# Optimization experiments

Hardware: AMD Instinct MI355X
Metric: run time of the kernel (lower is better)

The kernel has to match this reference:

```python
import jax, jax.numpy as jnp
import numpy as np
import math

B, C, H, W = 4, 256, 64, 64
NUM_HEADS = 4
GROUPS = 32
EPS = 1e-5


def setup_inputs() -> dict:
    key = jax.random.key(0)
    ks = jax.random.split(key, 7)
    x = jax.random.normal(ks[0], (B, C, H, W), dtype=jnp.float32)
    gn_w = jax.random.normal(ks[1], (C,), dtype=jnp.float32) * 0.02 + 1.0
    gn_b = jax.random.normal(ks[2], (C,), dtype=jnp.float32) * 0.02
    qkv_w = jax.random.normal(ks[3], (3 * C, C), dtype=jnp.float32) * (1.0 / math.sqrt(C))
    qkv_b = jax.random.normal(ks[4], (3 * C,), dtype=jnp.float32) * 0.02
    proj_w = jax.random.normal(ks[5], (C, C), dtype=jnp.float32) * (1.0 / math.sqrt(C))
    proj_b = jax.random.normal(ks[6], (C,), dtype=jnp.float32) * 0.02
    return {"x": x, "gn_w": gn_w, "gn_b": gn_b, "qkv_w": qkv_w,
            "qkv_b": qkv_b, "proj_w": proj_w, "proj_b": proj_b}


def reference(x, gn_w, gn_b, qkv_w, qkv_b, proj_w, proj_b):
    b, c, h, w = x.shape
    t = h * w
    xf = x.reshape(b, c, t)                       # [B, C, T]

    # GroupNorm(32, C) over (channels-in-group, T)
    xg = xf.reshape(b, GROUPS, c // GROUPS, t)
    mean = jnp.mean(xg, axis=(2, 3), keepdims=True)
    var = jnp.var(xg, axis=(2, 3), keepdims=True)
    xn = ((xg - mean) * jax.lax.rsqrt(var + EPS)).reshape(b, c, t)
    xn = xn * gn_w[None, :, None] + gn_b[None, :, None]

    # 1x1 conv QKV: [B, 3C, T]
    qkv = jnp.einsum('oc,bct->bot', qkv_w, xn) + qkv_b[None, :, None]

    nh = NUM_HEADS
    ch = c // nh
    q, k, v = jnp.split(qkv, 3, axis=1)           # each [B, H*ch, T]
    q = q.reshape(b * nh, ch, t)
    k = k.reshape(b * nh, ch, t)
    v = v.reshape(b * nh, ch, t)

    scale = 1.0 / math.sqrt(math.sqrt(ch))
    logits = jnp.einsum('bct,bcs->bts', q * scale, k * scale)   # [B*H, T, T]
    weight = jax.nn.softmax(logits.astype(jnp.float32), axis=-1).astype(logits.dtype)
    a = jnp.einsum('bts,bcs->bct', weight, v)     # [B*H, ch, T]
    a = a.reshape(b, c, t)

    hproj = jnp.einsum('oc,bct->bot', proj_w, a) + proj_b[None, :, None]
    return (xf + hproj).reshape(b, c, h, w)
```

## Files before the change

### kernel.cpp

```cpp
#include <hip/hip_runtime.h>
#include <cstdint>
#include <cstddef>

#define TT 4096
#define CCH 256

typedef __attribute__((ext_vector_type(8))) short short8;
typedef __attribute__((ext_vector_type(4))) float f32x4;

__device__ __forceinline__ float bf2f(unsigned int u){
  union { unsigned int i; float f; } v; v.i = u << 16; return v.f;
}
__device__ __forceinline__ unsigned short f2bf(float f){
  unsigned int x = __float_as_uint(f);
  x += 0x7fffu + ((x >> 16) & 1u);
  return (unsigned short)(x >> 16);
}
__device__ __forceinline__ unsigned short f2bf_t(float f){
  return (unsigned short)(__float_as_uint(f) >> 16);
}
__device__ __forceinline__ int sw(int row, int col){
  return (row << 6) + ((((col >> 3) ^ (row & 7)) << 3)) + (col & 7);
}

__global__ __launch_bounds__(256)
void wconv_gn(const float* __restrict__ qkv_w, const float* __restrict__ proj_w,
              const float* __restrict__ x,
              unsigned short* __restrict__ wq_bf, unsigned short* __restrict__ wp_bf,
              float* __restrict__ stats){
  int bid = blockIdx.x, tid = threadIdx.x;
  if (bid < 256){
    const float* src = (bid < 192) ? qkv_w : proj_w;
    unsigned short* dst = (bid < 192) ? wq_bf : wp_bf;
    int i = (bid < 192 ? bid : bid - 192) * 256 + tid;
    float4 u = *(const float4*)(src + (size_t)i * 4);
    ushort4 r; r.x = f2bf(u.x); r.y = f2bf(u.y); r.z = f2bf(u.z); r.w = f2bf(u.w);
    *(ushort4*)(dst + (size_t)i * 4) = r;
    return;
  }
  int sg = bid - 256;
  const float4* p = (const float4*)(x + (size_t)sg * 32768);
  float s = 0.f, sq = 0.f;
  #pragma unroll
  for (int it = 0; it < 32; ++it){
    float4 u = p[it * 256 + tid];
    s  += u.x + u.y + u.z + u.w;
    sq += u.x*u.x + u.y*u.y + u.z*u.z + u.w*u.w;
  }
  #pragma unroll
  for (int off = 32; off >= 1; off >>= 1){
    s  += __shfl_down(s, off);
    sq += __shfl_down(sq, off);
  }
  __shared__ float ls[4], lq[4];
  int w_ = tid >> 6, lane = tid & 63;
  if (lane == 0){ ls[w_] = s; lq[w_] = sq; }
  __syncthreads();
  if (tid == 0){
    float S = ls[0]+ls[1]+ls[2]+ls[3];
    float Q = lq[0]+lq[1]+lq[2]+lq[3];
    float mean = S * (1.f/32768.f);
    float var  = Q * (1.f/32768.f) - mean*mean;
    stats[2*sg]   = mean;
    stats[2*sg+1] = rsqrtf(var + 1e-5f);
  }
}

__global__ __launch_bounds__(256)
void gn_apply_t(const float* __restrict__ x, const float* __restrict__ gw,
                const float* __restrict__ gb, const float* __restrict__ stats,
                unsigned short* __restrict__ xnT){
  __shared__ unsigned short t_lds[64][72];
  int tid = threadIdx.x;
  int t0 = blockIdx.x << 6, c0 = blockIdx.y << 6, b = blockIdx.z;
  int t4 = (tid & 15) << 2, cr = tid >> 4;
  #pragma unroll
  for (int pass = 0; pass < 4; ++pass){
    int cl = (pass << 4) + cr;
    int c = c0 + cl;
    int sg = (b << 5) | (c >> 3);
    float mean = stats[2*sg], rstd = stats[2*sg+1];
    float sc = gw[c] * rstd;
    float sh = gb[c] - mean * sc;
    float4 u = *(const float4*)(x + ((size_t)(b*CCH + c))*TT + t0 + t4);
    t_lds[t4+0][cl] = f2bf(u.x*sc + sh);
    t_lds[t4+1][cl] = f2bf(u.y*sc + sh);
    t_lds[t4+2][cl] = f2bf(u.z*sc + sh);
    t_lds[t4+3][cl] = f2bf(u.w*sc + sh);
  }
  __syncthreads();
  #pragma unroll
  for (int pass = 0; pass < 2; ++pass){
    int chunk = (pass << 8) + tid;
    int row = chunk >> 3, c8 = (chunk & 7) << 3;
    *(uint4*)(xnT + ((size_t)b*TT + t0 + row)*256 + c0 + c8) = *(const uint4*)&t_lds[row][c8];
  }
}

__global__ __launch_bounds__(256)
void qkv_mfma(const unsigned short* __restrict__ wb, const float* __restrict__ bias,
              const unsigned short* __restrict__ xnT,
              unsigned short* __restrict__ qT, unsigned short* __restrict__ kT,
              unsigned short* __restrict__ vO){
  __shared__ unsigned short x_lds[4096];
  int tid = threadIdx.x;
  int w = tid >> 6, lane = tid & 63, quad = lane >> 4, l15 = lane & 15;
  int t0 = blockIdx.x << 6, o0 = blockIdx.y << 6, b = blockIdx.z;
  const unsigned short* xb = xnT + (size_t)b * TT * 256;
  const unsigned short* wrow = wb + (size_t)(o0 + (w << 4) + l15) * 256;
  f32x4 acc[4];
  #pragma unroll
  for (int nt = 0; nt < 4; ++nt) acc[nt] = (f32x4){0.f,0.f,0.f,0.f};
  for (int ks = 0; ks < 4; ++ks){
    int k0 = ks << 6;
    __syncthreads();
    #pragma unroll
    for (int pass = 0; pass < 2; ++pass){
      int chunk = (pass << 8) + tid;
      int row = chunk >> 3, c8 = (chunk & 7) << 3;
      *(uint4*)&x_lds[sw(row, c8)] = *(const uint4*)(xb + (size_t)(t0 + row)*256 + k0 + c8);
    }
    __syncthreads();
    short8 wa0 = *(const short8*)(wrow + k0 + (quad << 3));
    short8 wa1 = *(const short8*)(wrow + k0 + 32 + (quad << 3));
    #pragma unroll
    for (int nt = 0; nt < 4; ++nt){
      short8 xb0 = *(const short8*)&x_lds[sw((nt << 4) + l15, quad << 3)];
      short8 xb1 = *(const short8*)&x_lds[sw((nt << 4) + l15, 32 + (quad << 3))];
      acc[nt] = __builtin_amdgcn_mfma_f32_16x16x32_bf16(wa0, xb0, acc[nt], 0, 0, 0);
      acc[nt] = __builtin_amdgcn_mfma_f32_16x16x32_bf16(wa1, xb1, acc[nt], 0, 0, 0);
    }
  }
  int sec = blockIdx.y >> 2, h = blockIdx.y & 3, bh = (b << 2) | h;
  float bs[4];
  #pragma unroll
  for (int r = 0; r < 4; ++r) bs[r] = bias[o0 + (w << 4) + (quad << 2) + r];
  __syncthreads();
  if (sec < 2){
    float qsc = (sec == 0) ? 0.125f * 1.44269504f : 1.0f;
    #pragma unroll
    for (int nt = 0; nt < 4; ++nt){
      ushort4 pk;
      pk.x = f2bf((acc[nt][0] + bs[0]) * qsc);
      pk.y = f2bf((acc[nt][1] + bs[1]) * qsc);
      pk.z = f2bf((acc[nt][2] + bs[2]) * qsc);
      pk.w = f2bf((acc[nt][3] + bs[3]) * qsc);
      *(ushort4*)&x_lds[sw((nt << 4) + l15, (w << 4) + (quad << 2))] = pk;
    }
    __syncthreads();
    unsigned short* dst = (sec == 0) ? qT : kT;
    #pragma unroll
    for (int pass = 0; pass < 2; ++pass){
      int chunk = (pass << 8) + tid;
      int row = chunk >> 3, c8 = (chunk & 7) << 3;
      *(uint4*)(dst + ((size_t)bh*TT + t0 + row)*64 + c8) = *(const uint4*)&x_lds[sw(row, c8)];
    }
  } else {
    #pragma unroll
    for (int nt = 0; nt < 4; ++nt)
      #pragma unroll
      for (int r = 0; r < 4; ++r)
        x_lds[sw((w << 4) + (quad << 2) + r, (nt << 4) + l15)] = f2bf(acc[nt][r] + bs[r]);
    __syncthreads();
    #pragma unroll
    for (int pass = 0; pass < 2; ++pass){
      int chunk = (pass << 8) + tid;
      int row = chunk >> 3, c8 = (chunk & 7) << 3;
      *(uint4*)(vO + ((size_t)bh*64 + row)*TT + t0 + c8) = *(const uint4*)&x_lds[sw(row, c8)];
    }
  }
}

__global__ __launch_bounds__(256, 4)
void attn7(const unsigned short* __restrict__ qT, const unsigned short* __restrict__ kT,
           const unsigned short* __restrict__ vO, unsigned short* __restrict__ aT){
  __shared__ __align__(16) unsigned short k_lds[4096];
  __shared__ __align__(16) unsigned short v_lds[4096];
  __shared__ __align__(16) unsigned short p_lds[4096];
  int tid = threadIdx.x;
  int w = tid >> 6, lane = tid & 63, quad = lane >> 4, l15 = lane & 15;
  int bh = blockIdx.x & 15, qt6 = blockIdx.x >> 4;
  int t0 = qt6 << 6;
  const unsigned short* qg = qT + (size_t)bh * TT * 64;
  const unsigned short* kg = kT + (size_t)bh * TT * 64;
  const unsigned short* vg = vO + (size_t)bh * 64 * TT;
  int tw = t0 + (w << 4);

  int row0 = tid >> 3, c80 = (tid & 7) << 3;
  int row1 = row0 + 32;
  int soff0 = sw(row0, c80), soff1 = sw(row1, c80);

  short8 qf[2];
  qf[0] = *(const short8*)(qg + (size_t)(tw + l15)*64 + (quad << 3));
  qf[1] = *(const short8*)(qg + (size_t)(tw + l15)*64 + 32 + (quad << 3));

  f32x4 o_acc[4];
  #pragma unroll
  for (int ct = 0; ct < 4; ++ct) o_acc[ct] = (f32x4){0.f,0.f,0.f,0.f};
  float m_ = -1e30f, l_ = 0.f;

  uint4 kr0 = *(const uint4*)(kg + (size_t)row0*64 + c80);
  uint4 kr1 = *(const uint4*)(kg + (size_t)row1*64 + c80);
  uint4 vr0 = *(const uint4*)(vg + (size_t)row0*TT + c80);
  uint4 vr1 = *(const uint4*)(vg + (size_t)row1*TT + c80);

  for (int st = 0; st < 64; ++st){
    __syncthreads();
    *(uint4*)&k_lds[soff0] = kr0;
    *(uint4*)&k_lds[soff1] = kr1;
    *(uint4*)&v_lds[soff0] = vr0;
    *(uint4*)&v_lds[soff1] = vr1;
    if (st < 63){
      int sn = (st + 1) << 6;
      kr0 = *(const uint4*)(kg + (size_t)(sn + row0)*64 + c80);
      kr1 = *(const uint4*)(kg + (size_t)(sn + row1)*64 + c80);
      vr0 = *(const uint4*)(vg + (size_t)row0*TT + sn + c80);
      vr1 = *(const uint4*)(vg + (size_t)row1*TT + sn + c80);
    }
    __syncthreads();
    f32x4 sv[4];
    #pragma unroll
    for (int mt = 0; mt < 4; ++mt){
      short8 ka0 = *(const short8*)&k_lds[sw((mt << 4) + l15, quad << 3)];
      short8 ka1 = *(const short8*)&k_lds[sw((mt << 4) + l15, 32 + (quad << 3))];
      f32x4 z = (f32x4){0.f,0.f,0.f,0.f};
      z = __builtin_amdgcn_mfma_f32_16x16x32_bf16(ka0, qf[0], z, 0, 0, 0);
      z = __builtin_amdgcn_mfma_f32_16x16x32_bf16(ka1, qf[1], z, 0, 0, 0);
      sv[mt] = z;
    }
    float rm = -1e30f;
    #pragma unroll
    for (int mt = 0; mt < 4; ++mt)
      #pragma unroll
      for (int r = 0; r < 4; ++r) rm = fmaxf(rm, sv[mt][r]);
    rm = fmaxf(rm, __shfl_xor(rm, 16));
    rm = fmaxf(rm, __shfl_xor(rm, 32));
    float mnew = fmaxf(m_, rm);
    float alpha = exp2f(m_ - mnew);
    float rs = 0.f;
    int prow = (w << 4) + l15;
    #pragma unroll
    for (int mt = 0; mt < 4; ++mt){
      float p0 = exp2f(sv[mt][0] - mnew);
      float p1 = exp2f(sv[mt][1] - mnew);
      float p2 = exp2f(sv[mt][2] - mnew);
      float p3 = exp2f(sv[mt][3] - mnew);
      rs += (p0 + p1) + (p2 + p3);
      ushort4 pk; pk.x = f2bf_t(p0); pk.y = f2bf_t(p1); pk.z = f2bf_t(p2); pk.w = f2bf_t(p3);
      *(ushort4*)&p_lds[sw(prow, (mt << 4) + (quad << 2))] = pk;
    }
    rs += __shfl_xor(rs, 16);
    rs += __shfl_xor(rs, 32);
    l_ = l_*alpha + rs;
    m_ = mnew;
    #pragma unroll
    for (int ct = 0; ct < 4; ++ct)
      #pragma unroll
      for (int r = 0; r < 4; ++r) o_acc[ct][r] *= alpha;
    short8 pb0 = *(const short8*)&p_lds[sw(prow, quad << 3)];
    short8 pb1 = *(const short8*)&p_lds[sw(prow, 32 + (quad << 3))];
    #pragma unroll
    for (int ct = 0; ct < 4; ++ct){
      short8 va0 = *(const short8*)&v_lds[sw((ct << 4) + l15, quad << 3)];
      short8 va1 = *(const short8*)&v_lds[sw((ct << 4) + l15, 32 + (quad << 3))];
      o_acc[ct] = __builtin_amdgcn_mfma_f32_16x16x32_bf16(va0, pb0, o_acc[ct], 0, 0, 0);
      o_acc[ct] = __builtin_amdgcn_mfma_f32_16x16x32_bf16(va1, pb1, o_acc[ct], 0, 0, 0);
    }
  }
  __syncthreads();
  float ir = 1.f / l_;
  int prow = (w << 4) + l15;
  #pragma unroll
  for (int ct = 0; ct < 4; ++ct){
    ushort4 ok;
    ok.x = f2bf(o_acc[ct][0] * ir);
    ok.y = f2bf(o_acc[ct][1] * ir);
    ok.z = f2bf(o_acc[ct][2] * ir);
    ok.w = f2bf(o_acc[ct][3] * ir);
    *(ushort4*)&p_lds[sw(prow, (ct << 4) + (quad << 2))] = ok;
  }
  __syncthreads();
  size_t abase = ((size_t)(bh >> 2)*TT + t0)*256 + (size_t)(bh & 3)*64;
  #pragma unroll
  for (int pass = 0; pass < 2; ++pass){
    int chunk = (pass << 8) + tid;
    int row = chunk >> 3, c8 = (chunk & 7) << 3;
    *(uint4*)(aT + abase + (size_t)row*256 + c8) = *(const uint4*)&p_lds[sw(row, c8)];
  }
}

__global__ __launch_bounds__(256)
void proj_mfma(const unsigned short* __restrict__ wb, const float* __restrict__ bias,
               const unsigned short* __restrict__ aT, const float* __restrict__ x,
               float* __restrict__ out){
  __shared__ unsigned short x_lds[4096];
  int tid = threadIdx.x;
  int w = tid >> 6, lane = tid & 63, quad = lane >> 4, l15 = lane & 15;
  int t0 = blockIdx.x << 6, o0 = blockIdx.y << 6, b = blockIdx.z;
  const unsigned short* xb = aT + (size_t)b * TT * 256;
  const unsigned short* wrow = wb + (size_t)(o0 + (w << 4) + l15) * 256;
  f32x4 acc[4];
  #pragma unroll
  for (int nt = 0; nt < 4; ++nt) acc[nt] = (f32x4){0.f,0.f,0.f,0.f};
  for (int ks = 0; ks < 4; ++ks){
    int k0 = ks << 6;
    __syncthreads();
    #pragma unroll
    for (int pass = 0; pass < 2; ++pass){
      int chunk = (pass << 8) + tid;
      int row = chunk >> 3, c8 = (chunk & 7) << 3;
      *(uint4*)&x_lds[sw(row, c8)] = *(const uint4*)(xb + (size_t)(t0 + row)*256 + k0 + c8);
    }
    __syncthreads();
    short8 wa0 = *(const short8*)(wrow + k0 + (quad << 3));
    short8 wa1 = *(const short8*)(wrow + k0 + 32 + (quad << 3));
    #pragma unroll
    for (int nt = 0; nt < 4; ++nt){
      short8 xb0 = *(const short8*)&x_lds[sw((nt << 4) + l15, quad << 3)];
      short8 xb1 = *(const short8*)&x_lds[sw((nt << 4) + l15, 32 + (quad << 3))];
      acc[nt] = __builtin_amdgcn_mfma_f32_16x16x32_bf16(wa0, xb0, acc[nt], 0, 0, 0);
      acc[nt] = __builtin_amdgcn_mfma_f32_16x16x32_bf16(wa1, xb1, acc[nt], 0, 0, 0);
    }
  }
  #pragma unroll
  for (int r = 0; r < 4; ++r){
    int o = o0 + (w << 4) + (quad << 2) + r;
    float bsv = bias[o];
    #pragma unroll
    for (int nt = 0; nt < 4; ++nt){
      size_t idx = ((size_t)(b*CCH + o))*TT + t0 + (nt << 4) + l15;
      out[idx] = acc[nt][r] + bsv + x[idx];
    }
  }
}

extern "C" void kernel_launch(void* const* d_in, const int* in_sizes, int n_in,
                              void* d_out, int out_size, void* d_ws, size_t ws_size,
                              hipStream_t stream){
  const float* x      = (const float*)d_in[0];
  const float* gn_w   = (const float*)d_in[1];
  const float* gn_b   = (const float*)d_in[2];
  const float* qkv_w  = (const float*)d_in[3];
  const float* qkv_b  = (const float*)d_in[4];
  const float* proj_w = (const float*)d_in[5];
  const float* proj_b = (const float*)d_in[6];
  float* out = (float*)d_out;

  float* stats = (float*)d_ws;
  unsigned short* wq_bf = (unsigned short*)(stats + 1024);
  unsigned short* wp_bf = wq_bf + (size_t)768*256;
  unsigned short* xnT   = wp_bf + (size_t)256*256;
  unsigned short* qT    = xnT + (size_t)4*TT*256;
  unsigned short* kT    = qT  + (size_t)16*TT*64;
  unsigned short* vO    = kT  + (size_t)16*TT*64;
  unsigned short* aT    = vO  + (size_t)16*64*TT;

  wconv_gn<<<384, 256, 0, stream>>>(qkv_w, proj_w, x, wq_bf, wp_bf, stats);
  gn_apply_t<<<dim3(64, 4, 4), 256, 0, stream>>>(x, gn_w, gn_b, stats, xnT);
  qkv_mfma<<<dim3(64, 12, 4), 256, 0, stream>>>(wq_bf, qkv_b, xnT, qT, kT, vO);
  attn7<<<1024, 256, 0, stream>>>(qT, kT, vO, aT);
  proj_mfma<<<dim3(64, 4, 4), 256, 0, stream>>>(wp_bf, proj_b, aT, x, out);
}
```

Baseline: 247.8 us.

## Streamline attention softmax with lazy rescale, MFMA row sums and permlane reductions

Reworks the online-softmax inner loop of the attention kernel. The running max is only updated, and the accumulators rescaled, when any lane's new max exceeds the old by more than a threshold, chosen wave-wide via ballot. The row sum of P is computed with an MFMA against a ones vector instead of VALU adds and shuffles. Cross-lane max uses permlane swap instructions, P is packed with a hardware bf16 convert, and MFMA phases get raised scheduling priority. This cuts VALU and shuffle work, but the lazy max lets exponents grow up to 2^8 before rescaling and adds a branch.

Result: faster. 239.3 us (-3.5%).

```diff
diff --git a/kernel.cpp b/kernel.cpp
--- a/kernel.cpp
+++ b/kernel.cpp
@@ -21,6 +21,21 @@
 }
 __device__ __forceinline__ int sw(int row, int col){
   return (row << 6) + ((((col >> 3) ^ (row & 7)) << 3)) + (col & 7);
+}
+__device__ __forceinline__ float bfly_max16(float x){
+  unsigned a = __float_as_uint(x), b = a;
+  asm("v_permlane16_swap_b32 %0, %1" : "+v"(a), "+v"(b));
+  return fmaxf(__uint_as_float(a), __uint_as_float(b));
+}
+__device__ __forceinline__ float bfly_max32(float x){
+  unsigned a = __float_as_uint(x), b = a;
+  asm("v_permlane32_swap_b32 %0, %1" : "+v"(a), "+v"(b));
+  return fmaxf(__uint_as_float(a), __uint_as_float(b));
+}
+__device__ __forceinline__ unsigned cvt_pk_bf16(float lo, float hi){
+  unsigned r;
+  asm("v_cvt_pk_bf16_f32 %0, %1, %2" : "=v"(r) : "v"(lo), "v"(hi));
+  return r;
 }
 
 __global__ __launch_bounds__(256)
@@ -194,6 +209,10 @@
   qf[0] = *(const short8*)(qg + (size_t)(tw + l15)*64 + (quad << 3));
   qf[1] = *(const short8*)(qg + (size_t)(tw + l15)*64 + 32 + (quad << 3));
 
+  short8 ones;
+  #pragma unroll
+  for (int i = 0; i < 8; ++i) ones[i] = (short)0x3F80;
+
   f32x4 o_acc[4];
   #pragma unroll
   for (int ct = 0; ct < 4; ++ct) o_acc[ct] = (f32x4){0.f,0.f,0.f,0.f};
@@ -203,6 +222,8 @@
   uint4 kr1 = *(const uint4*)(kg + (size_t)row1*64 + c80);
   uint4 vr0 = *(const uint4*)(vg + (size_t)row0*TT + c80);
   uint4 vr1 = *(const uint4*)(vg + (size_t)row1*TT + c80);
+
+  int prow = (w << 4) + l15;
 
   for (int st = 0; st < 64; ++st){
     __syncthreads();
@@ -219,6 +240,7 @@
     }
     __syncthreads();
     f32x4 sv[4];
+    __builtin_amdgcn_s_setprio(1);
     #pragma unroll
     for (int mt = 0; mt < 4; ++mt){
       short8 ka0 = *(const short8*)&k_lds[sw((mt << 4) + l15, quad << 3)];
@@ -228,37 +250,40 @@
       z = __builtin_amdgcn_mfma_f32_16x16x32_bf16(ka1, qf[1], z, 0, 0, 0);
       sv[mt] = z;
     }
-    float rm = -1e30f;
-    #pragma unroll
-    for (int mt = 0; mt < 4; ++mt)
+    __builtin_amdgcn_s_setprio(0);
+    float rm = fmaxf(fmaxf(sv[0][0], sv[0][1]), fmaxf(sv[0][2], sv[0][3]));
+    #pragma unroll
+    for (int mt = 1; mt < 4; ++mt)
+      rm = fmaxf(rm, fmaxf(fmaxf(sv[mt][0], sv[mt][1]), fmaxf(sv[mt][2], sv[mt][3])));
+    rm = bfly_max16(rm);
+    rm = bfly_max32(rm);
+    float alpha = 1.0f;
+    if (__ballot(rm > m_ + 8.0f)){
+      float mnew = fmaxf(m_, rm);
+      alpha = exp2f(m_ - mnew);
+      m_ = mnew;
       #pragma unroll
-      for (int r = 0; r < 4; ++r) rm = fmaxf(rm, sv[mt][r]);
-    rm = fmaxf(rm, __shfl_xor(rm, 16));
-    rm = fmaxf(rm, __shfl_xor(rm, 32));
-    float mnew = fmaxf(m_, rm);
-    float alpha = exp2f(m_ - mnew);
-    float rs = 0.f;
-    int prow = (w << 4) + l15;
+      for (int ct = 0; ct < 4; ++ct)
+        #pragma unroll
+        for (int r = 0; r < 4; ++r) o_acc[ct][r] *= alpha;
+    }
     #pragma unroll
     for (int mt = 0; mt < 4; ++mt){
-      float p0 = exp2f(sv[mt][0] - mnew);
-      float p1 = exp2f(sv[mt][1] - mnew);
-      float p2 = exp2f(sv[mt][2] - mnew);
-      float p3 = exp2f(sv[mt][3] - mnew);
-      rs += (p0 + p1) + (p2 + p3);
-      ushort4 pk; pk.x = f2bf_t(p0); pk.y = f2bf_t(p1); pk.z = f2bf_t(p2); pk.w = f2bf_t(p3);
-      *(ushort4*)&p_lds[sw(prow, (mt << 4) + (quad << 2))] = pk;
-    }
-    rs += __shfl_xor(rs, 16);
-    rs += __shfl_xor(rs, 32);
-    l_ = l_*alpha + rs;
-    m_ = mnew;
-    #pragma unroll
-    for (int ct = 0; ct < 4; ++ct)
-      #pragma unroll
-      for (int r = 0; r < 4; ++r) o_acc[ct][r] *= alpha;
+      float p0 = exp2f(sv[mt][0] - m_);
+      float p1 = exp2f(sv[mt][1] - m_);
+      float p2 = exp2f(sv[mt][2] - m_);
+      float p3 = exp2f(sv[mt][3] - m_);
+      uint2 pkk;
+      pkk.x = cvt_pk_bf16(p0, p1);
+      pkk.y = cvt_pk_bf16(p2, p3);
+      *(uint2*)&p_lds[sw(prow, (mt << 4) + (quad << 2))] = pkk;
+    }
     short8 pb0 = *(const short8*)&p_lds[sw(prow, quad << 3)];
     short8 pb1 = *(const short8*)&p_lds[sw(prow, 32 + (quad << 3))];
+    __builtin_amdgcn_s_setprio(1);
+    f32x4 ls4 = (f32x4){0.f,0.f,0.f,0.f};
+    ls4 = __builtin_amdgcn_mfma_f32_16x16x32_bf16(ones, pb0, ls4, 0, 0, 0);
+    ls4 = __builtin_amdgcn_mfma_f32_16x16x32_bf16(ones, pb1, ls4, 0, 0, 0);
     #pragma unroll
     for (int ct = 0; ct < 4; ++ct){
       short8 va0 = *(const short8*)&v_lds[sw((ct << 4) + l15, quad << 3)];
@@ -266,10 +291,11 @@
       o_acc[ct] = __builtin_amdgcn_mfma_f32_16x16x32_bf16(va0, pb0, o_acc[ct], 0, 0, 0);
       o_acc[ct] = __builtin_amdgcn_mfma_f32_16x16x32_bf16(va1, pb1, o_acc[ct], 0, 0, 0);
     }
+    __builtin_amdgcn_s_setprio(0);
+    l_ = l_ * alpha + ls4[0];
   }
   __syncthreads();
   float ir = 1.f / l_;
-  int prow = (w << 4) + l15;
   #pragma unroll
   for (int ct = 0; ct < 4; ++ct){
     ushort4 ok;
```
